# Kernel tuning notes

Hardware: AMD Instinct MI355X
Metric: run time of the kernel (lower is better)

## Reference

```python
import jax, jax.numpy as jnp
import numpy as np

IN_FEATURES = 1024
HIDDEN_DIM = 1024
B, S = 4, 4096


def setup_inputs() -> dict:
    key = jax.random.key(0)
    ks = jax.random.split(key, 7)
    lim = 1.0 / np.sqrt(IN_FEATURES)
    x = jax.random.normal(ks[0], (B, S, IN_FEATURES), dtype=jnp.float32)
    Wq = jax.random.uniform(ks[1], (IN_FEATURES, HIDDEN_DIM), jnp.float32, -lim, lim)
    bq = jax.random.uniform(ks[2], (HIDDEN_DIM,), jnp.float32, -lim, lim)
    Wk = jax.random.uniform(ks[3], (IN_FEATURES, HIDDEN_DIM), jnp.float32, -lim, lim)
    bk = jax.random.uniform(ks[4], (HIDDEN_DIM,), jnp.float32, -lim, lim)
    Wv = jax.random.uniform(ks[5], (IN_FEATURES, HIDDEN_DIM), jnp.float32, -lim, lim)
    bv = jax.random.uniform(ks[6], (HIDDEN_DIM,), jnp.float32, -lim, lim)
    return {"x": x, "Wq": Wq, "bq": bq, "Wk": Wk, "bk": bk, "Wv": Wv, "bv": bv}


def reference(x, Wq, bq, Wk, bk, Wv, bv):
    # QKV projections: [B, S, H]
    q = jnp.einsum('bsf,fh->bsh', x, Wq) + bq
    k = jnp.einsum('bsf,fh->bsh', x, Wk) + bk
    v = jnp.einsum('bsf,fh->bsh', x, Wv) + bv
    scale = 1.0 / jnp.sqrt(jnp.asarray(q.shape[-1], dtype=q.dtype))
    scores = jnp.einsum('bqh,bkh->bqk', q, k) * scale  # [B, S, S]
    weights = jax.nn.softmax(scores, axis=-1)
    return jnp.einsum('bqk,bkh->bqh', weights, v)
```

## Files before the change

### kernel.cpp

```cpp
#include <hip/hip_runtime.h>

typedef _Float16 half_t;
typedef _Float16 half4_t __attribute__((ext_vector_type(4)));
typedef _Float16 half8_t __attribute__((ext_vector_type(8)));
typedef float float4_t __attribute__((ext_vector_type(4)));

#define S_LEN 4096
#define NB 4
#define H_DIM 1024

#define MFMA16(a, b, c) __builtin_amdgcn_mfma_f32_16x16x32_f16(a, b, c, 0, 0, 0)

__global__ __launch_bounds__(256) void wt_prep(
    const float* __restrict__ Wq, const float* __restrict__ Wk,
    const float* __restrict__ Wv, half_t* __restrict__ wth,
    half_t* __restrict__ wtl) {
  const int zi = blockIdx.z;
  const float* W = (zi == 0) ? Wq : (zi == 1) ? Wk : Wv;
  half_t* oh = wth + (size_t)zi * H_DIM * H_DIM;
  half_t* ol = wtl + (size_t)zi * H_DIM * H_DIM;
  const int h0 = blockIdx.x * 32, f0 = blockIdx.y * 32;
  __shared__ float Ws[32][33];
  const int t = threadIdx.x;
  const int c = t & 31, r8 = t >> 5;
#pragma unroll
  for (int rr = 0; rr < 4; rr++)
    Ws[r8 * 4 + rr][c] = W[(size_t)(f0 + r8 * 4 + rr) * H_DIM + h0 + c];
  __syncthreads();
#pragma unroll
  for (int rr = 0; rr < 4; rr++) {
    int h = r8 * 4 + rr;
    float v = Ws[c][h];
    half_t hi = (half_t)v;
    half_t lo = (half_t)(v - (float)hi);
    oh[(size_t)(h0 + h) * H_DIM + f0 + c] = hi;
    ol[(size_t)(h0 + h) * H_DIM + f0 + c] = lo;
  }
}

#define QKV_BK 64

__global__ __launch_bounds__(256, 2) void qkv_mfma(
    const float* __restrict__ x, const half_t* __restrict__ wth,
    const half_t* __restrict__ wtl, const float* __restrict__ bq,
    const float* __restrict__ bk, const float* __restrict__ bv,
    half_t* __restrict__ ws) {
  const int zi = blockIdx.z;
  const half_t* Ah_g = wth + (size_t)zi * H_DIM * H_DIM;
  const half_t* Al_g = wtl + (size_t)zi * H_DIM * H_DIM;
  const float* bias = (zi == 0) ? bq : (zi == 1) ? bk : bv;
  half_t* out = ws + (size_t)zi * ((size_t)NB * S_LEN * H_DIM);
  const int m0 = blockIdx.x * 128;
  const int n0 = blockIdx.y * 128;
  const int t = threadIdx.x;
  const int w = t >> 6, lane = t & 63, ln = lane & 15, quad = lane >> 4;

  __shared__ half_t Bs[16384];

  float4_t acc[2][8] = {};

  const int ss = t >> 1;
  const int fh = (t & 1) * 32;
  const int snt = ss >> 4, sln = ss & 15;

  for (int k0 = 0; k0 < H_DIM; k0 += QKV_BK) {
    half8_t ah[2][2], al[2][2];
#pragma unroll
    for (int i = 0; i < 2; i++) {
      const size_t arow =
          (size_t)(m0 + w * 32 + i * 16 + ln) * H_DIM + k0 + quad * 8;
#pragma unroll
      for (int k2 = 0; k2 < 2; k2++) {
        ah[i][k2] = *(const half8_t*)(Ah_g + arow + k2 * 32);
        al[i][k2] = *(const half8_t*)(Al_g + arow + k2 * 32);
      }
    }
    __syncthreads();
    {
      const float* xp = x + (size_t)(n0 + ss) * H_DIM + k0 + fh;
#pragma unroll
      for (int g = 0; g < 4; g++) {
        float4 v0 = *(const float4*)(xp + g * 8);
        float4 v1 = *(const float4*)(xp + g * 8 + 4);
        float vv[8] = {v0.x, v0.y, v0.z, v0.w, v1.x, v1.y, v1.z, v1.w};
        half8_t hhi, hlo;
#pragma unroll
        for (int j = 0; j < 8; j++) {
          half_t h = (half_t)vv[j];
          hhi[j] = h;
          hlo[j] = (half_t)(vv[j] - (float)h);
        }
        int f = fh + g * 8;
        int k2 = f >> 5, qd = (f >> 3) & 3;
        int base = ((k2 * 8 + snt) * 64 + qd * 16 + sln) * 8;
        *(half8_t*)&Bs[base] = hhi;
        *(half8_t*)&Bs[8192 + base] = hlo;
      }
    }
    __syncthreads();
#pragma unroll
    for (int k2 = 0; k2 < 2; k2++) {
#pragma unroll
      for (int nt = 0; nt < 8; nt++) {
        int base = ((k2 * 8 + nt) * 64 + lane) * 8;
        half8_t bh = *(const half8_t*)&Bs[base];
        half8_t bl = *(const half8_t*)&Bs[8192 + base];
        acc[0][nt] = MFMA16(ah[0][k2], bh, acc[0][nt]);
        acc[1][nt] = MFMA16(ah[1][k2], bh, acc[1][nt]);
        acc[0][nt] = MFMA16(al[0][k2], bh, acc[0][nt]);
        acc[1][nt] = MFMA16(al[1][k2], bh, acc[1][nt]);
        acc[0][nt] = MFMA16(ah[0][k2], bl, acc[0][nt]);
        acc[1][nt] = MFMA16(ah[1][k2], bl, acc[1][nt]);
      }
    }
  }

  const float oscale = (zi == 0) ? 0.03125f : 1.0f;
  float bb[2][4];
#pragma unroll
  for (int i = 0; i < 2; i++)
#pragma unroll
    for (int r = 0; r < 4; r++)
      bb[i][r] = bias[m0 + w * 32 + i * 16 + quad * 4 + r];

  if (zi < 2) {
#pragma unroll
    for (int i = 0; i < 2; i++)
#pragma unroll
      for (int nt = 0; nt < 8; nt++) {
        half4_t h4;
#pragma unroll
        for (int r = 0; r < 4; r++)
          h4[r] = (half_t)((acc[i][nt][r] + bb[i][r]) * oscale);
        size_t s = n0 + nt * 16 + ln;
        *(half4_t*)&out[s * H_DIM + m0 + w * 32 + i * 16 + quad * 4] = h4;
      }
  } else {
#pragma unroll
    for (int i = 0; i < 2; i++)
#pragma unroll
      for (int nt = 0; nt < 8; nt++) {
        int sf = n0 + nt * 16 + ln;
        int b = sf >> 12, si = sf & 4095;
#pragma unroll
        for (int r = 0; r < 4; r++) {
          int h = m0 + w * 32 + i * 16 + quad * 4 + r;
          out[((size_t)b * H_DIM + h) * S_LEN + si] =
              (half_t)(acc[i][nt][r] + bb[i][r]);
        }
      }
  }
}

#define TQ 64
#define TK 128

__global__ __launch_bounds__(512, 2) void flash_attn(
    const half_t* __restrict__ qw, const half_t* __restrict__ kw,
    const half_t* __restrict__ vt, float* __restrict__ out) {
  const int slot = blockIdx.x & 7;
  const int b = slot >> 1;
  const int qb = ((blockIdx.x >> 3) << 1) | (slot & 1);
  const int q0 = qb * TQ;
  const int t = threadIdx.x;
  const int w = t >> 6;
  const int lane = t & 63;
  const int ln = lane & 15;
  const int quad = lane >> 4;

  __shared__ half_t Qs[65536];
  __shared__ half_t Ps[8192];
  __shared__ float wmax[8][64];
  __shared__ float wl[8][64];
  __shared__ float mS[64], lS[64], aS[64];

  const half_t* qp = qw + ((size_t)b * S_LEN + q0) * H_DIM;
  const half_t* kbp = kw + (size_t)b * S_LEN * H_DIM;
  const half_t* vbt = vt + (size_t)b * H_DIM * S_LEN;

#pragma unroll
  for (int i = 0; i < 16; i++) {
    int flat = t * 8 + i * 4096;
    int r = flat >> 10, c = flat & 1023;
    int rs = r >> 4, lq = r & 15, ks = c >> 5, qd = (c >> 3) & 3;
    *(half8_t*)&Qs[((rs * 32 + ks) * 64 + qd * 16 + lq) * 8] =
        *(const half8_t*)&qp[(size_t)r * H_DIM + c];
  }
  if (t < 64) {
    mS[t] = -1e30f;
    lS[t] = 0.0f;
  }
  __syncthreads();

  float4_t O[4][8] = {};

  for (int kt = 0; kt < S_LEN; kt += TK) {
    float4_t s[4] = {};
    const half_t* kr = kbp + (size_t)(kt + w * 16 + ln) * H_DIM + quad * 8;
    half8_t kbuf[6];
#pragma unroll
    for (int d = 0; d < 6; d++) kbuf[d] = *(const half8_t*)(kr + d * 32);
#pragma unroll
    for (int ks = 0; ks < 32; ks++) {
      half8_t a0 = *(const half8_t*)&Qs[(ks * 64 + lane) * 8];
      half8_t a1 = *(const half8_t*)&Qs[16384 + (ks * 64 + lane) * 8];
      half8_t a2 = *(const half8_t*)&Qs[32768 + (ks * 64 + lane) * 8];
      half8_t a3 = *(const half8_t*)&Qs[49152 + (ks * 64 + lane) * 8];
      half8_t kc = kbuf[ks % 6];
      if (ks < 26) kbuf[ks % 6] = *(const half8_t*)(kr + (ks + 6) * 32);
      s[0] = MFMA16(a0, kc, s[0]);
      s[1] = MFMA16(a1, kc, s[1]);
      s[2] = MFMA16(a2, kc, s[2]);
      s[3] = MFMA16(a3, kc, s[3]);
    }

    const half_t* vbase = vbt + (size_t)(w * 128 + ln) * S_LEN + kt + quad * 8;
    half8_t vbuf[3][2];
#pragma unroll
    for (int u = 0; u < 2; u++)
#pragma unroll
      for (int c = 0; c < 2; c++)
        vbuf[u][c] =
            *(const half8_t*)(vbase + (size_t)u * 16 * S_LEN + c * 32);

    float rm[4][4];
#pragma unroll
    for (int rs = 0; rs < 4; rs++)
#pragma unroll
      for (int r = 0; r < 4; r++) rm[rs][r] = s[rs][r];
#pragma unroll
    for (int off = 1; off < 16; off <<= 1)
#pragma unroll
      for (int rs = 0; rs < 4; rs++)
#pragma unroll
        for (int r = 0; r < 4; r++)
          rm[rs][r] = fmaxf(rm[rs][r], __shfl_xor(rm[rs][r], off));
    if (ln == 0)
#pragma unroll
      for (int rs = 0; rs < 4; rs++)
#pragma unroll
        for (int r = 0; r < 4; r++)
          wmax[w][rs * 16 + quad * 4 + r] = rm[rs][r];
    __syncthreads();
    if (t < 64) {
      float nm = mS[t];
#pragma unroll
      for (int w2 = 0; w2 < 8; w2++) nm = fmaxf(nm, wmax[w2][t]);
      aS[t] = __expf(mS[t] - nm);
      mS[t] = nm;
    }
    __syncthreads();

    float nmv[4][4];
#pragma unroll
    for (int rs = 0; rs < 4; rs++)
#pragma unroll
      for (int r = 0; r < 4; r++) nmv[rs][r] = mS[rs * 16 + quad * 4 + r];
    const int pbase = (w >> 1) * 512 + (w & 1) * 256 + (ln >> 3) * 128 +
                      quad * 32 + (ln & 7);
    float pl[4][4];
#pragma unroll
    for (int rs = 0; rs < 4; rs++)
#pragma unroll
      for (int r = 0; r < 4; r++) {
        float p = __expf(s[rs][r] - nmv[rs][r]);
        pl[rs][r] = p;
        Ps[pbase + rs * 2048 + r * 8] = (half_t)p;
      }
#pragma unroll
    for (int off = 1; off < 16; off <<= 1)
#pragma unroll
      for (int rs = 0; rs < 4; rs++)
#pragma unroll
        for (int r = 0; r < 4; r++) pl[rs][r] += __shfl_xor(pl[rs][r], off);
    if (ln == 0)
#pragma unroll
      for (int rs = 0; rs < 4; rs++)
#pragma unroll
        for (int r = 0; r < 4; r++)
          wl[w][rs * 16 + quad * 4 + r] = pl[rs][r];
    __syncthreads();
    if (t < 64) {
      float s8 = 0.f;
#pragma unroll
      for (int w2 = 0; w2 < 8; w2++) s8 += wl[w2][t];
      lS[t] = lS[t] * aS[t] + s8;
    }

    float al[4][4];
#pragma unroll
    for (int rs = 0; rs < 4; rs++)
#pragma unroll
      for (int r = 0; r < 4; r++) al[rs][r] = aS[rs * 16 + quad * 4 + r];
#pragma unroll
    for (int rs = 0; rs < 4; rs++)
#pragma unroll
      for (int j = 0; j < 8; j++)
#pragma unroll
        for (int r = 0; r < 4; r++) O[rs][j][r] *= al[rs][r];

    half8_t pa[4][2];
#pragma unroll
    for (int u = 0; u < 16; u++) {
      const int kc2 = u >> 3, j = u & 7;
      if ((u & 7) == 0) {
#pragma unroll
        for (int rs = 0; rs < 4; rs++)
#pragma unroll
          for (int c = 0; c < 2; c++)
            pa[rs][c] =
                *(const half8_t*)&Ps[((rs * 4 + kc2 * 2 + c) * 64 + lane) * 8];
      }
      if (u < 14) {
        const int un = u + 2;
#pragma unroll
        for (int c = 0; c < 2; c++)
          vbuf[un % 3][c] = *(const half8_t*)(
              vbase + (size_t)(un & 7) * 16 * S_LEN +
              ((un >> 3) * 2 + c) * 32);
      }
#pragma unroll
      for (int c = 0; c < 2; c++)
#pragma unroll
        for (int rs = 0; rs < 4; rs++)
          O[rs][j] = MFMA16(pa[rs][c], vbuf[u % 3][c], O[rs][j]);
    }
  }

  __syncthreads();
  float il[4][4];
#pragma unroll
  for (int rs = 0; rs < 4; rs++)
#pragma unroll
    for (int r = 0; r < 4; r++) il[rs][r] = 1.0f / lS[rs * 16 + quad * 4 + r];
  float* ob = out + ((size_t)b * S_LEN + q0) * H_DIM + w * 128 + ln;
#pragma unroll
  for (int rs = 0; rs < 4; rs++)
#pragma unroll
    for (int j = 0; j < 8; j++)
#pragma unroll
      for (int r = 0; r < 4; r++)
        ob[(size_t)(rs * 16 + quad * 4 + r) * H_DIM + j * 16] =
            O[rs][j][r] * il[rs][r];
}

extern "C" void kernel_launch(void* const* d_in, const int* in_sizes, int n_in,
                              void* d_out, int out_size, void* d_ws,
                              size_t ws_size, hipStream_t stream) {
  const float* x = (const float*)d_in[0];
  const float* Wq = (const float*)d_in[1];
  const float* bq = (const float*)d_in[2];
  const float* Wk = (const float*)d_in[3];
  const float* bk = (const float*)d_in[4];
  const float* Wv = (const float*)d_in[5];
  const float* bv = (const float*)d_in[6];
  half_t* ws = (half_t*)d_ws;
  float* out = (float*)d_out;

  half_t* wth = (half_t*)d_out;
  half_t* wtl = wth + (size_t)3 * H_DIM * H_DIM;

  wt_prep<<<dim3(32, 32, 3), 256, 0, stream>>>(Wq, Wk, Wv, wth, wtl);

  qkv_mfma<<<dim3(8, 128, 3), 256, 0, stream>>>(x, wth, wtl, bq, bk, bv, ws);

  const half_t* qw = ws;
  const half_t* kw = ws + (size_t)NB * S_LEN * H_DIM;
  const half_t* vt = ws + 2 * (size_t)NB * S_LEN * H_DIM;
  flash_attn<<<dim3((S_LEN / TQ) * NB), 512, 0, stream>>>(qw, kw, vt, out);
}
```

Baseline: 1.112 ms.

## Keep softmax row stats in per-wave registers and prefetch next K tile

Each wave now redundantly computes the running max and sum for all 64 rows from the shared per-wave partials and broadcasts them with lane shuffles. This removes the single-wave shared mLS/aS bookkeeping and cuts the syncthreads per tile from three to two lighter LDS barriers. The next K tile's registers are prefetched right after the QK MFMA loop, and the PV loop is reorganised around a 4-deep V register ring. s_setprio raises priority around the MFMA blocks. The risks are extra shuffle work, higher register pressure at two waves per SIMD, and relying on the hand-written barrier for LDS ordering.

```diff
diff --git a/kernel.cpp b/kernel.cpp
--- a/kernel.cpp
+++ b/kernel.cpp
@@ -10,6 +10,12 @@
 #define H_DIM 1024
 
 #define MFMA16(a, b, c) __builtin_amdgcn_mfma_f32_16x16x32_f16(a, b, c, 0, 0, 0)
+
+#define BAR_LDS()                                      \
+  do {                                                 \
+    asm volatile("s_waitcnt lgkmcnt(0)" ::: "memory"); \
+    __builtin_amdgcn_s_barrier();                      \
+  } while (0)
 
 __global__ __launch_bounds__(256) void wt_prep(
     const float* __restrict__ Wq, const float* __restrict__ Wk,
@@ -172,11 +178,15 @@
   __shared__ half_t Ps[8192];
   __shared__ float wmax[8][64];
   __shared__ float wl[8][64];
-  __shared__ float mS[64], lS[64], aS[64];
 
   const half_t* qp = qw + ((size_t)b * S_LEN + q0) * H_DIM;
   const half_t* kbp = kw + (size_t)b * S_LEN * H_DIM;
   const half_t* vbt = vt + (size_t)b * H_DIM * S_LEN;
+
+  const half_t* kr = kbp + (size_t)(w * 16 + ln) * H_DIM + quad * 8;
+  half8_t kbuf[6];
+#pragma unroll
+  for (int d = 0; d < 6; d++) kbuf[d] = *(const half8_t*)(kr + d * 32);
 
 #pragma unroll
   for (int i = 0; i < 16; i++) {
@@ -186,20 +196,16 @@
     *(half8_t*)&Qs[((rs * 32 + ks) * 64 + qd * 16 + lq) * 8] =
         *(const half8_t*)&qp[(size_t)r * H_DIM + c];
   }
-  if (t < 64) {
-    mS[t] = -1e30f;
-    lS[t] = 0.0f;
-  }
-  __syncthreads();
+  BAR_LDS();
+
+  float m_l = -1e30f;
+  float l_l = 0.0f;
 
   float4_t O[4][8] = {};
 
   for (int kt = 0; kt < S_LEN; kt += TK) {
     float4_t s[4] = {};
-    const half_t* kr = kbp + (size_t)(kt + w * 16 + ln) * H_DIM + quad * 8;
-    half8_t kbuf[6];
-#pragma unroll
-    for (int d = 0; d < 6; d++) kbuf[d] = *(const half8_t*)(kr + d * 32);
+    __builtin_amdgcn_s_setprio(1);
 #pragma unroll
     for (int ks = 0; ks < 32; ks++) {
       half8_t a0 = *(const half8_t*)&Qs[(ks * 64 + lane) * 8];
@@ -213,15 +219,19 @@
       s[2] = MFMA16(a2, kc, s[2]);
       s[3] = MFMA16(a3, kc, s[3]);
     }
+    __builtin_amdgcn_s_setprio(0);
+
+    kr += (size_t)TK * H_DIM;
+    if (kt + TK < S_LEN) {
+#pragma unroll
+      for (int d = 0; d < 6; d++) kbuf[d] = *(const half8_t*)(kr + d * 32);
+    }
 
     const half_t* vbase = vbt + (size_t)(w * 128 + ln) * S_LEN + kt + quad * 8;
-    half8_t vbuf[3][2];
-#pragma unroll
-    for (int u = 0; u < 2; u++)
-#pragma unroll
-      for (int c = 0; c < 2; c++)
-        vbuf[u][c] =
-            *(const half8_t*)(vbase + (size_t)u * 16 * S_LEN + c * 32);
+    half8_t vr[4];
+#pragma unroll
+    for (int j = 0; j < 4; j++)
+      vr[j] = *(const half8_t*)(vbase + (size_t)j * 16 * S_LEN);
 
     float rm[4][4];
 #pragma unroll
@@ -241,21 +251,14 @@
 #pragma unroll
         for (int r = 0; r < 4; r++)
           wmax[w][rs * 16 + quad * 4 + r] = rm[rs][r];
-    __syncthreads();
-    if (t < 64) {
-      float nm = mS[t];
-#pragma unroll
-      for (int w2 = 0; w2 < 8; w2++) nm = fmaxf(nm, wmax[w2][t]);
-      aS[t] = __expf(mS[t] - nm);
-      mS[t] = nm;
-    }
-    __syncthreads();
-
-    float nmv[4][4];
-#pragma unroll
-    for (int rs = 0; rs < 4; rs++)
-#pragma unroll
-      for (int r = 0; r < 4; r++) nmv[rs][r] = mS[rs * 16 + quad * 4 + r];
+    BAR_LDS();
+
+    float nm_l = m_l;
+#pragma unroll
+    for (int w2 = 0; w2 < 8; w2++) nm_l = fmaxf(nm_l, wmax[w2][lane]);
+    float aS_l = __expf(m_l - nm_l);
+    m_l = nm_l;
+
     const int pbase = (w >> 1) * 512 + (w & 1) * 256 + (ln >> 3) * 128 +
                       quad * 32 + (ln & 7);
     float pl[4][4];
@@ -263,9 +266,14 @@
     for (int rs = 0; rs < 4; rs++)
 #pragma unroll
       for (int r = 0; r < 4; r++) {
-        float p = __expf(s[rs][r] - nmv[rs][r]);
+        const int q = rs * 16 + quad * 4 + r;
+        float nmq = __shfl(m_l, q);
+        float aq = __shfl(aS_l, q);
+        float p = __expf(s[rs][r] - nmq);
         pl[rs][r] = p;
         Ps[pbase + rs * 2048 + r * 8] = (half_t)p;
+#pragma unroll
+        for (int j = 0; j < 8; j++) O[rs][j][r] *= aq;
       }
 #pragma unroll
     for (int off = 1; off < 16; off <<= 1)
@@ -279,60 +287,45 @@
 #pragma unroll
         for (int r = 0; r < 4; r++)
           wl[w][rs * 16 + quad * 4 + r] = pl[rs][r];
-    __syncthreads();
-    if (t < 64) {
-      float s8 = 0.f;
-#pragma unroll
-      for (int w2 = 0; w2 < 8; w2++) s8 += wl[w2][t];
-      lS[t] = lS[t] * aS[t] + s8;
-    }
-
-    float al[4][4];
-#pragma unroll
-    for (int rs = 0; rs < 4; rs++)
-#pragma unroll
-      for (int r = 0; r < 4; r++) al[rs][r] = aS[rs * 16 + quad * 4 + r];
-#pragma unroll
-    for (int rs = 0; rs < 4; rs++)
-#pragma unroll
-      for (int j = 0; j < 8; j++)
-#pragma unroll
-        for (int r = 0; r < 4; r++) O[rs][j][r] *= al[rs][r];
-
-    half8_t pa[4][2];
-#pragma unroll
-    for (int u = 0; u < 16; u++) {
-      const int kc2 = u >> 3, j = u & 7;
-      if ((u & 7) == 0) {
+    BAR_LDS();
+
+    float s8_l = 0.f;
+#pragma unroll
+    for (int w2 = 0; w2 < 8; w2++) s8_l += wl[w2][lane];
+    l_l = l_l * aS_l + s8_l;
+
+#pragma unroll
+    for (int kc = 0; kc < 4; kc++) {
+      half8_t pa[4];
+#pragma unroll
+      for (int rs = 0; rs < 4; rs++)
+        pa[rs] = *(const half8_t*)&Ps[((rs * 4 + kc) * 64 + lane) * 8];
+      __builtin_amdgcn_s_setprio(1);
+#pragma unroll
+      for (int j = 0; j < 8; j++) {
+        half8_t vc = vr[j & 3];
+        const int jn = j + 4;
+        if (jn < 8) {
+          vr[j & 3] =
+              *(const half8_t*)(vbase + (size_t)jn * 16 * S_LEN + kc * 32);
+        } else if (kc < 3) {
+          vr[j & 3] = *(const half8_t*)(vbase + (size_t)(jn - 8) * 16 * S_LEN +
+                                        (kc + 1) * 32);
+        }
 #pragma unroll
         for (int rs = 0; rs < 4; rs++)
-#pragma unroll
-          for (int c = 0; c < 2; c++)
-            pa[rs][c] =
-                *(const half8_t*)&Ps[((rs * 4 + kc2 * 2 + c) * 64 + lane) * 8];
-      }
-      if (u < 14) {
-        const int un = u + 2;
-#pragma unroll
-        for (int c = 0; c < 2; c++)
-          vbuf[un % 3][c] = *(const half8_t*)(
-              vbase + (size_t)(un & 7) * 16 * S_LEN +
-              ((un >> 3) * 2 + c) * 32);
-      }
-#pragma unroll
-      for (int c = 0; c < 2; c++)
-#pragma unroll
-        for (int rs = 0; rs < 4; rs++)
-          O[rs][j] = MFMA16(pa[rs][c], vbuf[u % 3][c], O[rs][j]);
-    }
-  }
-
-  __syncthreads();
+          O[rs][j] = MFMA16(pa[rs], vc, O[rs][j]);
+      }
+      __builtin_amdgcn_s_setprio(0);
+    }
+  }
+
   float il[4][4];
 #pragma unroll
   for (int rs = 0; rs < 4; rs++)
 #pragma unroll
-    for (int r = 0; r < 4; r++) il[rs][r] = 1.0f / lS[rs * 16 + quad * 4 + r];
+    for (int r = 0; r < 4; r++)
+      il[rs][r] = 1.0f / __shfl(l_l, rs * 16 + quad * 4 + r);
   float* ob = out + ((size_t)b * S_LEN + q0) * H_DIM + w * 128 + ln;
 #pragma unroll
   for (int rs = 0; rs < 4; rs++)
```

Measured after the change: 1.075 ms. 1.03x faster.
